# Performance work log

Hardware: AMD Instinct MI355X
Metric: run time of the kernel (lower is better)

The kernel has to match this reference:

```python
import jax, jax.numpy as jnp
import numpy as np

B = 262144
D = 26  # lip_dim + pose_dim
OUT = 512


def setup_inputs() -> dict:
    key = jax.random.key(0)
    k1, k2 = jax.random.split(key)
    input = jax.random.normal(k1, (B, D), dtype=jnp.float32)
    weight = jax.random.normal(k2, (OUT, D), dtype=jnp.float32)
    return {"input": input, "weight": weight}


def reference(input, weight):
    # weight: [512, d]; reduced QR -> Q: [512, d]
    w = weight + 1e-8
    Q, _ = jnp.linalg.qr(w)
    # torch: sum(diag_embed(input) @ Q.T, dim=1) == input @ Q.T  -> [B, 512]
    out = jnp.einsum('bd,od->bo', input, Q)
    return out
```

## Files before the change

### kernel.cpp

```cpp
#include <hip/hip_runtime.h>
#include <math.h>

#define QR_M 512
#define QR_N 26
#define OUTC 512
#define LDP 30

using half8_t = __attribute__((ext_vector_type(8))) _Float16;
using f32x4   = __attribute__((ext_vector_type(4))) float;

__global__ __launch_bounds__(512) void qr_kernel(const float* __restrict__ w,
                                                 _Float16* __restrict__ qf) {
  const int tid  = threadIdx.x;
  const int lane = tid & 63;
  const int wid  = tid >> 6;

  __shared__ float As[QR_M][LDP];
  __shared__ float Gs[QR_N][LDP];
  __shared__ float Rt[QR_N][LDP];
  __shared__ float Gp[4][91][4];

  {
    const float2* wp = reinterpret_cast<const float2*>(w + (size_t)tid * QR_N);
    float2 v[13];
#pragma unroll
    for (int i = 0; i < 13; ++i) v[i] = wp[i];
#pragma unroll
    for (int i = 0; i < 13; ++i) {
      As[tid][2 * i]     = v[i].x + 1e-8f;
      As[tid][2 * i + 1] = v[i].y + 1e-8f;
    }
  }
  __syncthreads();

  if (tid < 364) {
    const int chunk = tid / 91;
    const int blk   = tid - chunk * 91;
    int cb = 0, rem = blk;
    while (rem >= 13 - cb) { rem -= 13 - cb; ++cb; }
    const int db = cb + rem;
    const int c0 = 2 * cb, d0 = 2 * db;
    float s00 = 0.f, s01 = 0.f, s10 = 0.f, s11 = 0.f;
    const int r0 = chunk * 128;
    for (int r = r0; r < r0 + 128; ++r) {
      const float2 ac = *reinterpret_cast<const float2*>(&As[r][c0]);
      const float2 ad = *reinterpret_cast<const float2*>(&As[r][d0]);
      s00 += ac.x * ad.x; s01 += ac.x * ad.y;
      s10 += ac.y * ad.x; s11 += ac.y * ad.y;
    }
    Gp[chunk][blk][0] = s00; Gp[chunk][blk][1] = s01;
    Gp[chunk][blk][2] = s10; Gp[chunk][blk][3] = s11;
  }
  __syncthreads();

  if (tid < 364) {
    const int blk = tid >> 2;
    const int v   = tid & 3;
    int cb = 0, rem = blk;
    while (rem >= 13 - cb) { rem -= 13 - cb; ++cb; }
    const int db = cb + rem;
    const float s = Gp[0][blk][v] + Gp[1][blk][v] + Gp[2][blk][v] + Gp[3][blk][v];
    const int c = 2 * cb + (v >> 1);
    const int d = 2 * db + (v & 1);
    Gs[c][d] = s;
    Gs[d][c] = s;
  }
  __syncthreads();

  if (wid == 0) {
    const int c  = lane;
    const int cm = (c < QR_N) ? c : (QR_N - 1);
    float gcol[QR_N], tcol[QR_N], rcol[QR_N];
#pragma unroll
    for (int r = 0; r < QR_N; ++r) gcol[r] = Gs[r][cm];
#pragma unroll
    for (int r = 0; r < QR_N; ++r) tcol[r] = As[r][cm];
#pragma unroll
    for (int r = 0; r < QR_N; ++r) rcol[r] = 0.0f;

#pragma unroll
    for (int j = 0; j < QR_N; ++j) {
      float tg = gcol[j];
#pragma unroll
      for (int r = 0; r < QR_N; ++r) {
        if (r < j) tg -= __shfl(rcol[r], j) * rcol[r];
      }
      const float nsq   = __shfl(tg, j);
      const float alpha = __shfl(tcol[j], j);
      const float norm  = sqrtf(nsq);
      const float beta  = (alpha >= 0.0f) ? -norm : norm;
      const float tau   = (beta - alpha) / beta;
      const float scale = 1.0f / (alpha - beta);
      const float wc    = (tg - beta * tcol[j]) * scale;
      const float tw    = (c > j) ? (tau * wc) : 0.0f;
      tcol[j] -= tw;
      rcol[j]  = (c == j) ? beta : tcol[j];
#pragma unroll
      for (int rr = 0; rr < QR_N; ++rr) {
        if (rr > j) {
          const float vtop = __shfl(tcol[rr], j) * scale;
          tcol[rr] -= tw * vtop;
        }
      }
      if (c >= j && c < QR_N) Rt[c][j] = rcol[j];
    }
  }
  __syncthreads();

  float rinv[QR_N];
#pragma unroll
  for (int cc = 0; cc < QR_N; ++cc) rinv[cc] = 1.0f / Rt[cc][cc];

  float y[QR_N];
#pragma unroll
  for (int cc = 0; cc < QR_N; ++cc) y[cc] = As[tid][cc];
#pragma unroll
  for (int cc = 0; cc < QR_N; ++cc) {
    float s = y[cc];
    int k = 0;
#pragma unroll
    for (; k + 1 < cc; k += 2) {
      const float2 rk = *reinterpret_cast<const float2*>(&Rt[cc][k]);
      s -= y[k] * rk.x + y[k + 1] * rk.y;
    }
    if (k < cc) s -= y[k] * Rt[cc][k];
    y[cc] = s * rinv[cc];
  }

  half8_t h0, h1, h2, h3;
#pragma unroll
  for (int e = 0; e < 8; ++e) h0[e] = (_Float16)y[e];
#pragma unroll
  for (int e = 0; e < 8; ++e) h1[e] = (_Float16)y[8 + e];
#pragma unroll
  for (int e = 0; e < 8; ++e) h2[e] = (_Float16)y[16 + e];
  h3[0] = (_Float16)y[24]; h3[1] = (_Float16)y[25];
#pragma unroll
  for (int e = 2; e < 8; ++e) h3[e] = (_Float16)0.0f;
  half8_t* qrow = reinterpret_cast<half8_t*>(qf + (size_t)tid * 32);
  qrow[0] = h0; qrow[1] = h1; qrow[2] = h2; qrow[3] = h3;
}

__global__ __launch_bounds__(256, 4) void dir_matmul(const float* __restrict__ x,
                                                     const _Float16* __restrict__ qf,
                                                     float* __restrict__ out,
                                                     int nblk32) {
  const int tid   = threadIdx.x;
  const int wid   = tid >> 6;
  const int l     = tid & 63;
  const int rloc  = l & 15;
  const int grp   = l >> 4;
  const int k0    = grp * 8;
  const int rhalf = (wid >> 1) * 16;
  const int chalf = (wid & 1) * 256;
  const int t2b   = (wid & 1) * 16;

  __shared__ float tile[4][16 * 132];
  float* tw = tile[wid];

  half8_t bq[16];
#pragma unroll
  for (int t2 = 0; t2 < 16; ++t2)
    bq[t2] = *reinterpret_cast<const half8_t*>(
        qf + (size_t)((t2b + t2) * 16 + rloc) * 32 + k0);

  for (int rb = blockIdx.x; rb < nblk32; rb += gridDim.x) {
    const int row = rb * 32 + rhalf + rloc;
    half8_t av;
    const float* xp = x + (size_t)row * QR_N + k0;
    if (grp < 3) {
#pragma unroll
      for (int e = 0; e < 4; ++e) {
        float2 v = *reinterpret_cast<const float2*>(xp + 2 * e);
        av[2 * e]     = (_Float16)v.x;
        av[2 * e + 1] = (_Float16)v.y;
      }
    } else {
      float2 v = *reinterpret_cast<const float2*>(xp);
      av[0] = (_Float16)v.x; av[1] = (_Float16)v.y;
#pragma unroll
      for (int e = 2; e < 8; ++e) av[e] = (_Float16)0.0f;
    }

#pragma unroll
    for (int cc = 0; cc < 2; ++cc) {
#pragma unroll
      for (int tt = 0; tt < 8; ++tt) {
        f32x4 acc = {0.0f, 0.0f, 0.0f, 0.0f};
        acc = __builtin_amdgcn_mfma_f32_16x16x32_f16(av, bq[cc * 8 + tt], acc, 0, 0, 0);
#pragma unroll
        for (int j = 0; j < 4; ++j)
          tw[(grp * 4 + j) * 132 + tt * 16 + rloc] = acc[j];
      }
      __syncthreads();
#pragma unroll
      for (int it = 0; it < 8; ++it) {
        const int r  = it * 2 + (l >> 5);
        const int cg = l & 31;
        f32x4 v = *reinterpret_cast<const f32x4*>(&tw[r * 132 + 4 * cg]);
        *reinterpret_cast<f32x4*>(
            out + (size_t)(rb * 32 + rhalf + r) * OUTC + chalf + cc * 128 + 4 * cg) = v;
      }
      __syncthreads();
    }
  }
}

extern "C" void kernel_launch(void* const* d_in, const int* in_sizes, int n_in,
                              void* d_out, int out_size, void* d_ws, size_t ws_size,
                              hipStream_t stream) {
  const float* input  = (const float*)d_in[0];
  const float* weight = (const float*)d_in[1];
  float* out = (float*)d_out;
  _Float16* qf = (_Float16*)d_ws;

  const int B = in_sizes[0] / QR_N;
  const int nblk32 = B / 32;

  qr_kernel<<<1, 512, 0, stream>>>(weight, qf);
  dir_matmul<<<2048, 256, 0, stream>>>(input, qf, out, nblk32);
}
```

Baseline: 135.0 us.

## Fuse QR into matmul kernel, recomputing Q redundantly per block

Merges the single-block QR kernel and the matmul kernel into one launch. Each of 512 blocks recomputes the Gram matrix, Cholesky-style QR and triangular solve, and keeps Q in shared memory instead of writing it to a workspace. This removes one kernel launch and the serialized single-block QR stage before the matmul. In exchange every block repeats the QR work (reading the weights from global), and the grid drops from 2048 to 512 blocks with lower occupancy bounds.

```diff
diff --git a/kernel.cpp b/kernel.cpp
--- a/kernel.cpp
+++ b/kernel.cpp
@@ -9,31 +9,33 @@
 using half8_t = __attribute__((ext_vector_type(8))) _Float16;
 using f32x4   = __attribute__((ext_vector_type(4))) float;
 
-__global__ __launch_bounds__(512) void qr_kernel(const float* __restrict__ w,
-                                                 _Float16* __restrict__ qf) {
-  const int tid  = threadIdx.x;
-  const int lane = tid & 63;
-  const int wid  = tid >> 6;
-
-  __shared__ float As[QR_M][LDP];
+__global__ __launch_bounds__(256, 2) void fused_dir(const float* __restrict__ w,
+                                                    const float* __restrict__ x,
+                                                    float* __restrict__ out,
+                                                    int nblk32) {
+  const int tid = threadIdx.x;
+  const int l   = tid & 63;
+  const int wid = tid >> 6;
+
   __shared__ float Gs[QR_N][LDP];
   __shared__ float Rt[QR_N][LDP];
-  __shared__ float Gp[4][91][4];
-
+  __shared__ float Gp[2][91][4];
+  __shared__ __align__(16) _Float16 Qs[QR_M][32];
+  __shared__ float tile[4][16 * 132];
+
+  float a0[QR_N], a1[QR_N];
   {
-    const float2* wp = reinterpret_cast<const float2*>(w + (size_t)tid * QR_N);
-    float2 v[13];
-#pragma unroll
-    for (int i = 0; i < 13; ++i) v[i] = wp[i];
+    const float2* w0 = reinterpret_cast<const float2*>(w + (size_t)tid * QR_N);
+    const float2* w1 = reinterpret_cast<const float2*>(w + (size_t)(tid + 256) * QR_N);
 #pragma unroll
     for (int i = 0; i < 13; ++i) {
-      As[tid][2 * i]     = v[i].x + 1e-8f;
-      As[tid][2 * i + 1] = v[i].y + 1e-8f;
-    }
-  }
-  __syncthreads();
-
-  if (tid < 364) {
+      const float2 v0 = w0[i], v1 = w1[i];
+      a0[2 * i]     = v0.x + 1e-8f; a0[2 * i + 1] = v0.y + 1e-8f;
+      a1[2 * i]     = v1.x + 1e-8f; a1[2 * i + 1] = v1.y + 1e-8f;
+    }
+  }
+
+  if (tid < 182) {
     const int chunk = tid / 91;
     const int blk   = tid - chunk * 91;
     int cb = 0, rem = blk;
@@ -41,10 +43,11 @@
     const int db = cb + rem;
     const int c0 = 2 * cb, d0 = 2 * db;
     float s00 = 0.f, s01 = 0.f, s10 = 0.f, s11 = 0.f;
-    const int r0 = chunk * 128;
-    for (int r = r0; r < r0 + 128; ++r) {
-      const float2 ac = *reinterpret_cast<const float2*>(&As[r][c0]);
-      const float2 ad = *reinterpret_cast<const float2*>(&As[r][d0]);
+    const float* wr = w + (size_t)chunk * 256 * QR_N;
+    for (int r = 0; r < 256; ++r) {
+      float2 ac = *reinterpret_cast<const float2*>(wr + r * QR_N + c0);
+      float2 ad = *reinterpret_cast<const float2*>(wr + r * QR_N + d0);
+      ac.x += 1e-8f; ac.y += 1e-8f; ad.x += 1e-8f; ad.y += 1e-8f;
       s00 += ac.x * ad.x; s01 += ac.x * ad.y;
       s10 += ac.y * ad.x; s11 += ac.y * ad.y;
     }
@@ -53,28 +56,29 @@
   }
   __syncthreads();
 
-  if (tid < 364) {
-    const int blk = tid >> 2;
-    const int v   = tid & 3;
-    int cb = 0, rem = blk;
+  if (tid < 91) {
+    int cb = 0, rem = tid;
     while (rem >= 13 - cb) { rem -= 13 - cb; ++cb; }
     const int db = cb + rem;
-    const float s = Gp[0][blk][v] + Gp[1][blk][v] + Gp[2][blk][v] + Gp[3][blk][v];
-    const int c = 2 * cb + (v >> 1);
-    const int d = 2 * db + (v & 1);
-    Gs[c][d] = s;
-    Gs[d][c] = s;
+#pragma unroll
+    for (int v = 0; v < 4; ++v) {
+      const float s = Gp[0][tid][v] + Gp[1][tid][v];
+      const int c = 2 * cb + (v >> 1);
+      const int d = 2 * db + (v & 1);
+      Gs[c][d] = s;
+      Gs[d][c] = s;
+    }
   }
   __syncthreads();
 
   if (wid == 0) {
-    const int c  = lane;
+    const int c  = l;
     const int cm = (c < QR_N) ? c : (QR_N - 1);
     float gcol[QR_N], tcol[QR_N], rcol[QR_N];
 #pragma unroll
     for (int r = 0; r < QR_N; ++r) gcol[r] = Gs[r][cm];
 #pragma unroll
-    for (int r = 0; r < QR_N; ++r) tcol[r] = As[r][cm];
+    for (int r = 0; r < QR_N; ++r) tcol[r] = w[r * QR_N + cm] + 1e-8f;
 #pragma unroll
     for (int r = 0; r < QR_N; ++r) rcol[r] = 0.0f;
 
@@ -107,62 +111,68 @@
   }
   __syncthreads();
 
-  float rinv[QR_N];
-#pragma unroll
-  for (int cc = 0; cc < QR_N; ++cc) rinv[cc] = 1.0f / Rt[cc][cc];
-
-  float y[QR_N];
-#pragma unroll
-  for (int cc = 0; cc < QR_N; ++cc) y[cc] = As[tid][cc];
-#pragma unroll
-  for (int cc = 0; cc < QR_N; ++cc) {
-    float s = y[cc];
-    int k = 0;
-#pragma unroll
-    for (; k + 1 < cc; k += 2) {
-      const float2 rk = *reinterpret_cast<const float2*>(&Rt[cc][k]);
-      s -= y[k] * rk.x + y[k + 1] * rk.y;
-    }
-    if (k < cc) s -= y[k] * Rt[cc][k];
-    y[cc] = s * rinv[cc];
-  }
-
-  half8_t h0, h1, h2, h3;
-#pragma unroll
-  for (int e = 0; e < 8; ++e) h0[e] = (_Float16)y[e];
-#pragma unroll
-  for (int e = 0; e < 8; ++e) h1[e] = (_Float16)y[8 + e];
-#pragma unroll
-  for (int e = 0; e < 8; ++e) h2[e] = (_Float16)y[16 + e];
-  h3[0] = (_Float16)y[24]; h3[1] = (_Float16)y[25];
-#pragma unroll
-  for (int e = 2; e < 8; ++e) h3[e] = (_Float16)0.0f;
-  half8_t* qrow = reinterpret_cast<half8_t*>(qf + (size_t)tid * 32);
-  qrow[0] = h0; qrow[1] = h1; qrow[2] = h2; qrow[3] = h3;
-}
-
-__global__ __launch_bounds__(256, 4) void dir_matmul(const float* __restrict__ x,
-                                                     const _Float16* __restrict__ qf,
-                                                     float* __restrict__ out,
-                                                     int nblk32) {
-  const int tid   = threadIdx.x;
-  const int wid   = tid >> 6;
-  const int l     = tid & 63;
+  {
+    float rinv[QR_N];
+#pragma unroll
+    for (int cc = 0; cc < QR_N; ++cc) rinv[cc] = 1.0f / Rt[cc][cc];
+
+    float y0[QR_N], y1[QR_N];
+#pragma unroll
+    for (int cc = 0; cc < QR_N; ++cc) { y0[cc] = a0[cc]; y1[cc] = a1[cc]; }
+#pragma unroll
+    for (int cc = 0; cc < QR_N; ++cc) {
+      float s0 = y0[cc], s1 = y1[cc];
+      int k = 0;
+#pragma unroll
+      for (; k + 1 < cc; k += 2) {
+        const float2 rk = *reinterpret_cast<const float2*>(&Rt[cc][k]);
+        s0 -= y0[k] * rk.x + y0[k + 1] * rk.y;
+        s1 -= y1[k] * rk.x + y1[k + 1] * rk.y;
+      }
+      if (k < cc) { const float rk = Rt[cc][k]; s0 -= y0[k] * rk; s1 -= y1[k] * rk; }
+      y0[cc] = s0 * rinv[cc];
+      y1[cc] = s1 * rinv[cc];
+    }
+
+    half8_t h[4];
+#pragma unroll
+    for (int e = 0; e < 8; ++e) h[0][e] = (_Float16)y0[e];
+#pragma unroll
+    for (int e = 0; e < 8; ++e) h[1][e] = (_Float16)y0[8 + e];
+#pragma unroll
+    for (int e = 0; e < 8; ++e) h[2][e] = (_Float16)y0[16 + e];
+    h[3][0] = (_Float16)y0[24]; h[3][1] = (_Float16)y0[25];
+#pragma unroll
+    for (int e = 2; e < 8; ++e) h[3][e] = (_Float16)0.0f;
+    half8_t* q0 = reinterpret_cast<half8_t*>(&Qs[tid][0]);
+    q0[0] = h[0]; q0[1] = h[1]; q0[2] = h[2]; q0[3] = h[3];
+
+#pragma unroll
+    for (int e = 0; e < 8; ++e) h[0][e] = (_Float16)y1[e];
+#pragma unroll
+    for (int e = 0; e < 8; ++e) h[1][e] = (_Float16)y1[8 + e];
+#pragma unroll
+    for (int e = 0; e < 8; ++e) h[2][e] = (_Float16)y1[16 + e];
+    h[3][0] = (_Float16)y1[24]; h[3][1] = (_Float16)y1[25];
+#pragma unroll
+    for (int e = 2; e < 8; ++e) h[3][e] = (_Float16)0.0f;
+    half8_t* q1 = reinterpret_cast<half8_t*>(&Qs[tid + 256][0]);
+    q1[0] = h[0]; q1[1] = h[1]; q1[2] = h[2]; q1[3] = h[3];
+  }
+  __syncthreads();
+
   const int rloc  = l & 15;
   const int grp   = l >> 4;
   const int k0    = grp * 8;
   const int rhalf = (wid >> 1) * 16;
   const int chalf = (wid & 1) * 256;
   const int t2b   = (wid & 1) * 16;
-
-  __shared__ float tile[4][16 * 132];
   float* tw = tile[wid];
 
   half8_t bq[16];
 #pragma unroll
   for (int t2 = 0; t2 < 16; ++t2)
-    bq[t2] = *reinterpret_cast<const half8_t*>(
-        qf + (size_t)((t2b + t2) * 16 + rloc) * 32 + k0);
+    bq[t2] = *reinterpret_cast<const half8_t*>(&Qs[(t2b + t2) * 16 + rloc][k0]);
 
   for (int rb = blockIdx.x; rb < nblk32; rb += gridDim.x) {
     const int row = rb * 32 + rhalf + rloc;
@@ -212,11 +222,9 @@
   const float* input  = (const float*)d_in[0];
   const float* weight = (const float*)d_in[1];
   float* out = (float*)d_out;
-  _Float16* qf = (_Float16*)d_ws;
 
   const int B = in_sizes[0] / QR_N;
   const int nblk32 = B / 32;
 
-  qr_kernel<<<1, 512, 0, stream>>>(weight, qf);
-  dir_matmul<<<2048, 256, 0, stream>>>(input, qf, out, nblk32);
+  fused_dir<<<512, 256, 0, stream>>>(weight, input, out, nblk32);
 }
```

New measurement: 146.1 us. 8.3% more time.

## Split QR into parallel Gram partials and apply R inverse inside matmul

Applied to the files above, without the earlier changes.

Instead of forming Q explicitly in a single-block kernel, the Gram matrix is computed by 16 parallel blocks, a one-wave kernel factors it and inverts R, and the main matmul computes x·R^-1 with an extra small MFMA before multiplying by W (cast to fp16 on the fly). This shortens the serial single-block prologue that sat ahead of the big output-writing kernel. It adds a third launch, an extra MFMA stage per tile with fp16 rounding of the intermediate, and halves the matmul grid.

```diff
diff --git a/kernel.cpp b/kernel.cpp
--- a/kernel.cpp
+++ b/kernel.cpp
@@ -9,140 +9,108 @@
 using half8_t = __attribute__((ext_vector_type(8))) _Float16;
 using f32x4   = __attribute__((ext_vector_type(4))) float;
 
-__global__ __launch_bounds__(512) void qr_kernel(const float* __restrict__ w,
-                                                 _Float16* __restrict__ qf) {
-  const int tid  = threadIdx.x;
-  const int lane = tid & 63;
-  const int wid  = tid >> 6;
-
-  __shared__ float As[QR_M][LDP];
+__global__ __launch_bounds__(448) void gram_part(const float* __restrict__ w,
+                                                 float* __restrict__ gp) {
+  __shared__ float Ab[32][27];
+  const int tid = threadIdx.x;
+  const int b   = blockIdx.x;
+  if (tid < 416) {
+    const int r  = tid / 13;
+    const int c2 = tid - r * 13;
+    const float2 v = *reinterpret_cast<const float2*>(
+        w + (size_t)(b * 32 + r) * QR_N + 2 * c2);
+    Ab[r][2 * c2]     = v.x + 1e-8f;
+    Ab[r][2 * c2 + 1] = v.y + 1e-8f;
+  }
+  __syncthreads();
+  if (tid < 351) {
+    int cb = 0, rem = tid;
+    while (rem >= QR_N - cb) { rem -= QR_N - cb; ++cb; }
+    const int d = cb + rem;
+    float s = 0.0f;
+#pragma unroll
+    for (int r = 0; r < 32; ++r) s += Ab[r][cb] * Ab[r][d];
+    gp[b * 351 + tid] = s;
+  }
+}
+
+__global__ __launch_bounds__(64) void qr_small(const float* __restrict__ w,
+                                               const float* __restrict__ gp,
+                                               _Float16* __restrict__ rinv16) {
   __shared__ float Gs[QR_N][LDP];
-  __shared__ float Rt[QR_N][LDP];
-  __shared__ float Gp[4][91][4];
-
-  {
-    const float2* wp = reinterpret_cast<const float2*>(w + (size_t)tid * QR_N);
-    float2 v[13];
-#pragma unroll
-    for (int i = 0; i < 13; ++i) v[i] = wp[i];
-#pragma unroll
-    for (int i = 0; i < 13; ++i) {
-      As[tid][2 * i]     = v[i].x + 1e-8f;
-      As[tid][2 * i + 1] = v[i].y + 1e-8f;
+  const int l = threadIdx.x;
+
+#pragma unroll
+  for (int s = 0; s < 6; ++s) {
+    const int p = l + 64 * s;
+    if (p < 351) {
+      float acc = 0.0f;
+#pragma unroll
+      for (int b = 0; b < 16; ++b) acc += gp[b * 351 + p];
+      int cb = 0, rem = p;
+      while (rem >= QR_N - cb) { rem -= QR_N - cb; ++cb; }
+      const int d = cb + rem;
+      Gs[cb][d] = acc;
+      Gs[d][cb] = acc;
     }
   }
   __syncthreads();
 
-  if (tid < 364) {
-    const int chunk = tid / 91;
-    const int blk   = tid - chunk * 91;
-    int cb = 0, rem = blk;
-    while (rem >= 13 - cb) { rem -= 13 - cb; ++cb; }
-    const int db = cb + rem;
-    const int c0 = 2 * cb, d0 = 2 * db;
-    float s00 = 0.f, s01 = 0.f, s10 = 0.f, s11 = 0.f;
-    const int r0 = chunk * 128;
-    for (int r = r0; r < r0 + 128; ++r) {
-      const float2 ac = *reinterpret_cast<const float2*>(&As[r][c0]);
-      const float2 ad = *reinterpret_cast<const float2*>(&As[r][d0]);
-      s00 += ac.x * ad.x; s01 += ac.x * ad.y;
-      s10 += ac.y * ad.x; s11 += ac.y * ad.y;
-    }
-    Gp[chunk][blk][0] = s00; Gp[chunk][blk][1] = s01;
-    Gp[chunk][blk][2] = s10; Gp[chunk][blk][3] = s11;
-  }
-  __syncthreads();
-
-  if (tid < 364) {
-    const int blk = tid >> 2;
-    const int v   = tid & 3;
-    int cb = 0, rem = blk;
-    while (rem >= 13 - cb) { rem -= 13 - cb; ++cb; }
-    const int db = cb + rem;
-    const float s = Gp[0][blk][v] + Gp[1][blk][v] + Gp[2][blk][v] + Gp[3][blk][v];
-    const int c = 2 * cb + (v >> 1);
-    const int d = 2 * db + (v & 1);
-    Gs[c][d] = s;
-    Gs[d][c] = s;
-  }
-  __syncthreads();
-
-  if (wid == 0) {
-    const int c  = lane;
-    const int cm = (c < QR_N) ? c : (QR_N - 1);
-    float gcol[QR_N], tcol[QR_N], rcol[QR_N];
-#pragma unroll
-    for (int r = 0; r < QR_N; ++r) gcol[r] = Gs[r][cm];
-#pragma unroll
-    for (int r = 0; r < QR_N; ++r) tcol[r] = As[r][cm];
-#pragma unroll
-    for (int r = 0; r < QR_N; ++r) rcol[r] = 0.0f;
-
-#pragma unroll
-    for (int j = 0; j < QR_N; ++j) {
-      float tg = gcol[j];
-#pragma unroll
-      for (int r = 0; r < QR_N; ++r) {
-        if (r < j) tg -= __shfl(rcol[r], j) * rcol[r];
-      }
-      const float nsq   = __shfl(tg, j);
-      const float alpha = __shfl(tcol[j], j);
-      const float norm  = sqrtf(nsq);
-      const float beta  = (alpha >= 0.0f) ? -norm : norm;
-      const float tau   = (beta - alpha) / beta;
-      const float scale = 1.0f / (alpha - beta);
-      const float wc    = (tg - beta * tcol[j]) * scale;
-      const float tw    = (c > j) ? (tau * wc) : 0.0f;
-      tcol[j] -= tw;
-      rcol[j]  = (c == j) ? beta : tcol[j];
-#pragma unroll
-      for (int rr = 0; rr < QR_N; ++rr) {
-        if (rr > j) {
-          const float vtop = __shfl(tcol[rr], j) * scale;
-          tcol[rr] -= tw * vtop;
-        }
-      }
-      if (c >= j && c < QR_N) Rt[c][j] = rcol[j];
-    }
-  }
-  __syncthreads();
-
-  float rinv[QR_N];
-#pragma unroll
-  for (int cc = 0; cc < QR_N; ++cc) rinv[cc] = 1.0f / Rt[cc][cc];
-
-  float y[QR_N];
-#pragma unroll
-  for (int cc = 0; cc < QR_N; ++cc) y[cc] = As[tid][cc];
-#pragma unroll
-  for (int cc = 0; cc < QR_N; ++cc) {
-    float s = y[cc];
-    int k = 0;
-#pragma unroll
-    for (; k + 1 < cc; k += 2) {
-      const float2 rk = *reinterpret_cast<const float2*>(&Rt[cc][k]);
-      s -= y[k] * rk.x + y[k + 1] * rk.y;
-    }
-    if (k < cc) s -= y[k] * Rt[cc][k];
-    y[cc] = s * rinv[cc];
-  }
-
-  half8_t h0, h1, h2, h3;
-#pragma unroll
-  for (int e = 0; e < 8; ++e) h0[e] = (_Float16)y[e];
-#pragma unroll
-  for (int e = 0; e < 8; ++e) h1[e] = (_Float16)y[8 + e];
-#pragma unroll
-  for (int e = 0; e < 8; ++e) h2[e] = (_Float16)y[16 + e];
-  h3[0] = (_Float16)y[24]; h3[1] = (_Float16)y[25];
-#pragma unroll
-  for (int e = 2; e < 8; ++e) h3[e] = (_Float16)0.0f;
-  half8_t* qrow = reinterpret_cast<half8_t*>(qf + (size_t)tid * 32);
-  qrow[0] = h0; qrow[1] = h1; qrow[2] = h2; qrow[3] = h3;
+  const int c  = l;
+  const int cm = (c < QR_N) ? c : (QR_N - 1);
+  float gcol[QR_N], tcol[QR_N], rcol[QR_N];
+#pragma unroll
+  for (int r = 0; r < QR_N; ++r) gcol[r] = Gs[r][cm];
+#pragma unroll
+  for (int r = 0; r < QR_N; ++r) tcol[r] = w[r * QR_N + cm] + 1e-8f;
+#pragma unroll
+  for (int r = 0; r < QR_N; ++r) rcol[r] = 0.0f;
+
+#pragma unroll
+  for (int j = 0; j < QR_N; ++j) {
+    float tg = gcol[j];
+#pragma unroll
+    for (int r = 0; r < QR_N; ++r) {
+      if (r < j) tg -= __shfl(rcol[r], j) * rcol[r];
+    }
+    const float nsq   = __shfl(tg, j);
+    const float alpha = __shfl(tcol[j], j);
+    const float norm  = sqrtf(nsq);
+    const float beta  = (alpha >= 0.0f) ? -norm : norm;
+    const float tau   = (beta - alpha) / beta;
+    const float scale = 1.0f / (alpha - beta);
+    const float wc    = (tg - beta * tcol[j]) * scale;
+    const float tw    = (c > j) ? (tau * wc) : 0.0f;
+    tcol[j] -= tw;
+    rcol[j]  = (c == j) ? beta : tcol[j];
+#pragma unroll
+    for (int rr = 0; rr < QR_N; ++rr) {
+      if (rr > j) {
+        const float vtop = __shfl(tcol[rr], j) * scale;
+        tcol[rr] -= tw * vtop;
+      }
+    }
+  }
+
+  float z[QR_N];
+#pragma unroll
+  for (int k = QR_N - 1; k >= 0; --k) {
+    float s = (c == k) ? 1.0f : 0.0f;
+#pragma unroll
+    for (int m = k + 1; m < QR_N; ++m) s -= __shfl(rcol[k], m) * z[m];
+    z[k] = s / __shfl(rcol[k], k);
+  }
+  if (c < 32) {
+#pragma unroll
+    for (int k = 0; k < QR_N; ++k) rinv16[k * 32 + c] = (_Float16)z[k];
+#pragma unroll
+    for (int k = QR_N; k < 32; ++k) rinv16[k * 32 + c] = (_Float16)0.0f;
+  }
 }
 
 __global__ __launch_bounds__(256, 4) void dir_matmul(const float* __restrict__ x,
-                                                     const _Float16* __restrict__ qf,
+                                                     const float* __restrict__ w,
+                                                     const _Float16* __restrict__ rinv16,
                                                      float* __restrict__ out,
                                                      int nblk32) {
   const int tid   = threadIdx.x;
@@ -156,13 +124,34 @@
   const int t2b   = (wid & 1) * 16;
 
   __shared__ float tile[4][16 * 132];
+  __shared__ __align__(16) _Float16 xs[4][16][40];
   float* tw = tile[wid];
 
+  half8_t rv[2];
+#pragma unroll
+  for (int t = 0; t < 2; ++t)
+    rv[t] = *reinterpret_cast<const half8_t*>(rinv16 + (size_t)(t * 16 + rloc) * 32 + k0);
+
   half8_t bq[16];
 #pragma unroll
-  for (int t2 = 0; t2 < 16; ++t2)
-    bq[t2] = *reinterpret_cast<const half8_t*>(
-        qf + (size_t)((t2b + t2) * 16 + rloc) * 32 + k0);
+  for (int t2 = 0; t2 < 16; ++t2) {
+    const float* wp = w + (size_t)((t2b + t2) * 16 + rloc) * QR_N + k0;
+    half8_t h;
+    if (grp < 3) {
+#pragma unroll
+      for (int e = 0; e < 4; ++e) {
+        const float2 v = *reinterpret_cast<const float2*>(wp + 2 * e);
+        h[2 * e]     = (_Float16)(v.x + 1e-8f);
+        h[2 * e + 1] = (_Float16)(v.y + 1e-8f);
+      }
+    } else {
+      const float2 v = *reinterpret_cast<const float2*>(wp);
+      h[0] = (_Float16)(v.x + 1e-8f); h[1] = (_Float16)(v.y + 1e-8f);
+#pragma unroll
+      for (int e = 2; e < 8; ++e) h[e] = (_Float16)0.0f;
+    }
+    bq[t2] = h;
+  }
 
   for (int rb = blockIdx.x; rb < nblk32; rb += gridDim.x) {
     const int row = rb * 32 + rhalf + rloc;
@@ -171,23 +160,33 @@
     if (grp < 3) {
 #pragma unroll
       for (int e = 0; e < 4; ++e) {
-        float2 v = *reinterpret_cast<const float2*>(xp + 2 * e);
+        const float2 v = *reinterpret_cast<const float2*>(xp + 2 * e);
         av[2 * e]     = (_Float16)v.x;
         av[2 * e + 1] = (_Float16)v.y;
       }
     } else {
-      float2 v = *reinterpret_cast<const float2*>(xp);
+      const float2 v = *reinterpret_cast<const float2*>(xp);
       av[0] = (_Float16)v.x; av[1] = (_Float16)v.y;
 #pragma unroll
       for (int e = 2; e < 8; ++e) av[e] = (_Float16)0.0f;
     }
 
+    f32x4 p0 = {0.f, 0.f, 0.f, 0.f}, p1 = {0.f, 0.f, 0.f, 0.f};
+    p0 = __builtin_amdgcn_mfma_f32_16x16x32_f16(av, rv[0], p0, 0, 0, 0);
+    p1 = __builtin_amdgcn_mfma_f32_16x16x32_f16(av, rv[1], p1, 0, 0, 0);
+#pragma unroll
+    for (int j = 0; j < 4; ++j) {
+      xs[wid][grp * 4 + j][rloc]      = (_Float16)p0[j];
+      xs[wid][grp * 4 + j][16 + rloc] = (_Float16)p1[j];
+    }
+    const half8_t av2 = *reinterpret_cast<const half8_t*>(&xs[wid][rloc][k0]);
+
 #pragma unroll
     for (int cc = 0; cc < 2; ++cc) {
 #pragma unroll
       for (int tt = 0; tt < 8; ++tt) {
-        f32x4 acc = {0.0f, 0.0f, 0.0f, 0.0f};
-        acc = __builtin_amdgcn_mfma_f32_16x16x32_f16(av, bq[cc * 8 + tt], acc, 0, 0, 0);
+        f32x4 acc = {0.f, 0.f, 0.f, 0.f};
+        acc = __builtin_amdgcn_mfma_f32_16x16x32_f16(av2, bq[cc * 8 + tt], acc, 0, 0, 0);
 #pragma unroll
         for (int j = 0; j < 4; ++j)
           tw[(grp * 4 + j) * 132 + tt * 16 + rloc] = acc[j];
@@ -197,7 +196,7 @@
       for (int it = 0; it < 8; ++it) {
         const int r  = it * 2 + (l >> 5);
         const int cg = l & 31;
-        f32x4 v = *reinterpret_cast<const f32x4*>(&tw[r * 132 + 4 * cg]);
+        const f32x4 v = *reinterpret_cast<const f32x4*>(&tw[r * 132 + 4 * cg]);
         *reinterpret_cast<f32x4*>(
             out + (size_t)(rb * 32 + rhalf + r) * OUTC + chalf + cc * 128 + 4 * cg) = v;
       }
@@ -212,11 +211,14 @@
   const float* input  = (const float*)d_in[0];
   const float* weight = (const float*)d_in[1];
   float* out = (float*)d_out;
-  _Float16* qf = (_Float16*)d_ws;
+
+  float*     gp     = (float*)d_ws;
+  _Float16*  rinv16 = (_Float16*)((char*)d_ws + 24576);
 
   const int B = in_sizes[0] / QR_N;
   const int nblk32 = B / 32;
 
-  qr_kernel<<<1, 512, 0, stream>>>(weight, qf);
-  dir_matmul<<<2048, 256, 0, stream>>>(input, qf, out, nblk32);
-}
+  gram_part<<<16, 448, 0, stream>>>(weight, gp);
+  qr_small<<<1, 64, 0, stream>>>(weight, gp, rinv16);
+  dir_matmul<<<1024, 256, 0, stream>>>(input, weight, rinv16, out, nblk32);
+}
```

Result: slower. 143.7 us (+6.5%).
